# Kernel optimization log

Hardware: AMD Instinct MI355X
Metric: run time of the kernel (lower is better)

## Reference

```python
import jax, jax.numpy as jnp
import numpy as np

EPS = 1e-05
DILATION = 1

def setup_inputs() -> dict:
    key = jax.random.key(0)
    k1, k2 = jax.random.split(key)
    B, T, D, K = 4, 4096, 2048, 4
    x = jax.random.normal(k1, (B, T, D), dtype=jnp.float32)
    norm_weight = jnp.ones((D,), dtype=jnp.float32)
    conv_weight = jax.random.normal(k2, (D, 1, K), dtype=jnp.float32) * (1.0 / np.sqrt(K))
    return {"x": x, "norm_weight": norm_weight, "conv_weight": conv_weight}

def reference(x, norm_weight, conv_weight):
    B, T, D = x.shape
    K = conv_weight.shape[-1]
    pad = (K - 1) * DILATION
    # RMSNorm over last dim
    ms = jnp.mean(jnp.square(x), axis=-1, keepdims=True)
    y = x * jax.lax.rsqrt(ms + EPS) * norm_weight
    # to channel-first [B, D, T]
    y = jnp.transpose(y, (0, 2, 1))
    # causal depthwise conv: left-pad (K-1)*dilation, valid conv == torch pad-both + slice[:T]
    y = jax.lax.conv_general_dilated(
        y, conv_weight,
        window_strides=(1,),
        padding=[(pad, 0)],
        rhs_dilation=(DILATION,),
        dimension_numbers=("NCH", "OIH", "NCH"),
        feature_group_count=D,
    )
    # SiLU then back to [B, T, D]
    y = y * jax.nn.sigmoid(y)
    return jnp.transpose(y, (0, 2, 1))
```

## Files before the change

### kernel.cpp

```cpp
#include <hip/hip_runtime.h>
#include <math.h>

#define D_DIM 2048
#define T_DIM 4096
#define K_DIM 4
#define TT 32

__global__ __launch_bounds__(256) void rms_kernel(const float* __restrict__ x,
                                                  float* __restrict__ inv_rms) {
    const int wave = blockIdx.x * 4 + (threadIdx.x >> 6);
    const int lane = threadIdx.x & 63;
    const float4* xr = (const float4*)(x + (size_t)wave * D_DIM);
    float s = 0.f;
#pragma unroll
    for (int i = 0; i < (D_DIM / 4) / 64; ++i) {
        float4 v = xr[lane + i * 64];
        s += v.x * v.x + v.y * v.y + v.z * v.z + v.w * v.w;
    }
#pragma unroll
    for (int off = 32; off > 0; off >>= 1) s += __shfl_down(s, off, 64);
    if (lane == 0) inv_rms[wave] = rsqrtf(s * (1.0f / D_DIM) + 1e-5f);
}

__global__ __launch_bounds__(256) void conv_kernel(const float* __restrict__ x,
                                                   const float* __restrict__ g,
                                                   const float* __restrict__ w,
                                                   const float* __restrict__ inv_rms,
                                                   float* __restrict__ out) {
    const int b  = blockIdx.z;
    const int t0 = blockIdx.y * TT;
    const int d0 = blockIdx.x * 1024 + threadIdx.x * 4;

    __shared__ float s_r[TT + 3];
    if (threadIdx.x < TT + 3) {
        const int t = t0 - 3 + (int)threadIdx.x;
        s_r[threadIdx.x] = (t >= 0) ? inv_rms[(size_t)b * T_DIM + t] : 0.f;
    }
    __syncthreads();

    const float4 gv = *(const float4*)(g + d0);
    float wgt[4][4];
#pragma unroll
    for (int j = 0; j < 4; ++j) {
        float4 wv = *(const float4*)(w + (size_t)(d0 + j) * K_DIM);
        wgt[j][0] = wv.x; wgt[j][1] = wv.y; wgt[j][2] = wv.z; wgt[j][3] = wv.w;
    }

    const float* xb = x   + ((size_t)b * T_DIM) * D_DIM + d0;
    float*       ob = out + ((size_t)b * T_DIM) * D_DIM + d0;

    float win[3][4];
#pragma unroll
    for (int p = 0; p < 3; ++p) {
        const int t = t0 - 3 + p;
        if (t >= 0) {
            float4 xv = *(const float4*)(xb + (size_t)t * D_DIM);
            const float r = s_r[p];
            win[p][0] = xv.x * r * gv.x;
            win[p][1] = xv.y * r * gv.y;
            win[p][2] = xv.z * r * gv.z;
            win[p][3] = xv.w * r * gv.w;
        } else {
            win[p][0] = win[p][1] = win[p][2] = win[p][3] = 0.f;
        }
    }

#pragma unroll
    for (int i = 0; i < TT; ++i) {
        const int t = t0 + i;
        float4 xv = *(const float4*)(xb + (size_t)t * D_DIM);
        const float r = s_r[i + 3];
        float yn[4] = { xv.x * r * gv.x, xv.y * r * gv.y,
                        xv.z * r * gv.z, xv.w * r * gv.w };
        float4 o;
        float* op = &o.x;
#pragma unroll
        for (int j = 0; j < 4; ++j) {
            const float v = wgt[j][0] * win[0][j] + wgt[j][1] * win[1][j] +
                            wgt[j][2] * win[2][j] + wgt[j][3] * yn[j];
            op[j] = v / (1.f + __expf(-v));
        }
        *(float4*)(ob + (size_t)t * D_DIM) = o;
#pragma unroll
        for (int j = 0; j < 4; ++j) {
            win[0][j] = win[1][j];
            win[1][j] = win[2][j];
            win[2][j] = yn[j];
        }
    }
}

extern "C" void kernel_launch(void* const* d_in, const int* in_sizes, int n_in,
                              void* d_out, int out_size, void* d_ws, size_t ws_size,
                              hipStream_t stream) {
    const float* x = (const float*)d_in[0];
    const float* g = (const float*)d_in[1];
    const float* w = (const float*)d_in[2];
    float* out = (float*)d_out;

    const int total = in_sizes[0];
    const int rows  = total / D_DIM;
    const int B     = rows / T_DIM;

    float* inv_rms = (float*)d_ws;

    rms_kernel<<<rows / 4, 256, 0, stream>>>(x, inv_rms);

    dim3 grid(D_DIM / 1024, T_DIM / TT, B);
    conv_kernel<<<grid, 256, 0, stream>>>(x, g, w, inv_rms, out);
}
```

Before: 254.5 us.

## Fuse RMSNorm reduction into conv kernel with full-row blocks held in registers

```diff
diff --git a/kernel.cpp b/kernel.cpp
--- a/kernel.cpp
+++ b/kernel.cpp
@@ -4,41 +4,66 @@
 #define D_DIM 2048
 #define T_DIM 4096
 #define K_DIM 4
-#define TT 32
+#define TT    16
+#define NROW  (TT + 3)
+#define NTHREADS (D_DIM / 4)
+#define NWAVES  (NTHREADS / 64)
 
-__global__ __launch_bounds__(256) void rms_kernel(const float* __restrict__ x,
-                                                  float* __restrict__ inv_rms) {
-    const int wave = blockIdx.x * 4 + (threadIdx.x >> 6);
-    const int lane = threadIdx.x & 63;
-    const float4* xr = (const float4*)(x + (size_t)wave * D_DIM);
-    float s = 0.f;
+__global__ __launch_bounds__(NTHREADS) void fused_kernel(
+    const float* __restrict__ x,
+    const float* __restrict__ g,
+    const float* __restrict__ w,
+    float* __restrict__ out)
+{
+    const int b    = blockIdx.y;
+    const int t0   = blockIdx.x * TT;
+    const int tid  = threadIdx.x;
+    const int d0   = tid * 4;
+    const int lane = tid & 63;
+    const int wid  = tid >> 6;
+
+    __shared__ float s_part[NROW][NWAVES];
+    __shared__ float s_inv[NROW];
+
+    const float* xb = x + ((size_t)b * T_DIM) * D_DIM + d0;
+
+    float4 xv[NROW];
 #pragma unroll
-    for (int i = 0; i < (D_DIM / 4) / 64; ++i) {
-        float4 v = xr[lane + i * 64];
-        s += v.x * v.x + v.y * v.y + v.z * v.z + v.w * v.w;
+    for (int r = 0; r < NROW; ++r) {
+        const int t = t0 - 3 + r;
+        if (t >= 0) {
+            xv[r] = *(const float4*)(xb + (size_t)t * D_DIM);
+        } else {
+            xv[r] = make_float4(0.f, 0.f, 0.f, 0.f);
+        }
     }
 #pragma unroll
-    for (int off = 32; off > 0; off >>= 1) s += __shfl_down(s, off, 64);
-    if (lane == 0) inv_rms[wave] = rsqrtf(s * (1.0f / D_DIM) + 1e-5f);
-}
-
-__global__ __launch_bounds__(256) void conv_kernel(const float* __restrict__ x,
-                                                   const float* __restrict__ g,
-                                                   const float* __restrict__ w,
-                                                   const float* __restrict__ inv_rms,
-                                                   float* __restrict__ out) {
-    const int b  = blockIdx.z;
-    const int t0 = blockIdx.y * TT;
-    const int d0 = blockIdx.x * 1024 + threadIdx.x * 4;
-
-    __shared__ float s_r[TT + 3];
-    if (threadIdx.x < TT + 3) {
-        const int t = t0 - 3 + (int)threadIdx.x;
-        s_r[threadIdx.x] = (t >= 0) ? inv_rms[(size_t)b * T_DIM + t] : 0.f;
+    for (int r = 0; r < NROW; ++r) {
+        float p = xv[r].x * xv[r].x + xv[r].y * xv[r].y +
+                  xv[r].z * xv[r].z + xv[r].w * xv[r].w;
+#pragma unroll
+        for (int off = 32; off > 0; off >>= 1) p += __shfl_down(p, off, 64);
+        if (lane == 0) s_part[r][wid] = p;
+    }
+    __syncthreads();
+    if (tid < NROW) {
+        float s = 0.f;
+#pragma unroll
+        for (int wv = 0; wv < NWAVES; ++wv) s += s_part[tid][wv];
+        s_inv[tid] = rsqrtf(s * (1.0f / D_DIM) + 1e-5f);
     }
     __syncthreads();
 
     const float4 gv = *(const float4*)(g + d0);
+#pragma unroll
+    for (int r = 0; r < NROW; ++r) {
+        const float rv = s_inv[r];
+        xv[r].x *= rv * gv.x;
+        xv[r].y *= rv * gv.y;
+        xv[r].z *= rv * gv.z;
+        xv[r].w *= rv * gv.w;
+    }
+
     float wgt[4][4];
 #pragma unroll
     for (int j = 0; j < 4; ++j) {
@@ -46,47 +71,20 @@
         wgt[j][0] = wv.x; wgt[j][1] = wv.y; wgt[j][2] = wv.z; wgt[j][3] = wv.w;
     }
 
-    const float* xb = x   + ((size_t)b * T_DIM) * D_DIM + d0;
-    float*       ob = out + ((size_t)b * T_DIM) * D_DIM + d0;
-
-    float win[3][4];
-#pragma unroll
-    for (int p = 0; p < 3; ++p) {
-        const int t = t0 - 3 + p;
-        if (t >= 0) {
-            float4 xv = *(const float4*)(xb + (size_t)t * D_DIM);
-            const float r = s_r[p];
-            win[p][0] = xv.x * r * gv.x;
-            win[p][1] = xv.y * r * gv.y;
-            win[p][2] = xv.z * r * gv.z;
-            win[p][3] = xv.w * r * gv.w;
-        } else {
-            win[p][0] = win[p][1] = win[p][2] = win[p][3] = 0.f;
-        }
-    }
-
+    float* ob = out + ((size_t)b * T_DIM) * D_DIM + d0;
 #pragma unroll
     for (int i = 0; i < TT; ++i) {
-        const int t = t0 + i;
-        float4 xv = *(const float4*)(xb + (size_t)t * D_DIM);
-        const float r = s_r[i + 3];
-        float yn[4] = { xv.x * r * gv.x, xv.y * r * gv.y,
-                        xv.z * r * gv.z, xv.w * r * gv.w };
         float4 o;
         float* op = &o.x;
 #pragma unroll
         for (int j = 0; j < 4; ++j) {
-            const float v = wgt[j][0] * win[0][j] + wgt[j][1] * win[1][j] +
-                            wgt[j][2] * win[2][j] + wgt[j][3] * yn[j];
-            op[j] = v / (1.f + __expf(-v));
+            const float v = wgt[j][0] * ((const float*)&xv[i    ])[j]
+                          + wgt[j][1] * ((const float*)&xv[i + 1])[j]
+                          + wgt[j][2] * ((const float*)&xv[i + 2])[j]
+                          + wgt[j][3] * ((const float*)&xv[i + 3])[j];
+            op[j] = v * __builtin_amdgcn_rcpf(1.f + __expf(-v));
         }
-        *(float4*)(ob + (size_t)t * D_DIM) = o;
-#pragma unroll
-        for (int j = 0; j < 4; ++j) {
-            win[0][j] = win[1][j];
-            win[1][j] = win[2][j];
-            win[2][j] = yn[j];
-        }
+        *(float4*)(ob + (size_t)(t0 + i) * D_DIM) = o;
     }
 }
 
@@ -102,10 +100,6 @@
     const int rows  = total / D_DIM;
     const int B     = rows / T_DIM;
 
-    float* inv_rms = (float*)d_ws;
-
-    rms_kernel<<<rows / 4, 256, 0, stream>>>(x, inv_rms);
-
-    dim3 grid(D_DIM / 1024, T_DIM / TT, B);
-    conv_kernel<<<grid, 256, 0, stream>>>(x, g, w, inv_rms, out);
+    dim3 grid(T_DIM / TT, B);
+    fused_kernel<<<grid, NTHREADS, 0, stream>>>(x, g, w, out);
 }
```

After: 241.1 us. -5.3%, faster.
